# Kernel optimization log

Hardware: AMD Instinct MI355X
Metric: run time of the kernel (lower is better)

Reference implementation:

```python
import jax, jax.numpy as jnp
import numpy as np

N = 65536      # total nodes (512 graphs x 128 agents)
E = 524288     # total edges (avg degree 8)
NPG = 128      # nodes per graph
OBS = 256      # dim_in_node + dim_in_u
HID = 512      # hidden_dim
MID = 256      # dim_mid
LSTM = 256     # dim_lstm_out
DOUT = 128     # dim_out
DLAST = 128    # dim_last
RFM = 256      # rfm_hidden_dim
LH = 256       # last_hidden
ACT = 8        # act_dims


def setup_inputs() -> dict:
    key = jax.random.key(0)
    ks = jax.random.split(key, 30)

    def rn(k, shape, fan_in):
        return jax.random.normal(k, shape, jnp.float32) * (1.0 / np.sqrt(fan_in))

    src = jax.random.randint(ks[3], (E,), 0, N, jnp.int32)
    # keep edges inside each 128-node graph (batched-graph semantics)
    dst = (src // NPG) * NPG + jax.random.randint(ks[4], (E,), 0, NPG, jnp.int32)

    inp = {
        "obs": jax.random.normal(ks[0], (N, OBS), jnp.float32),
        "h0": jax.random.normal(ks[1], (N, LSTM), jnp.float32) * 0.1,
        "c0": jax.random.normal(ks[2], (N, LSTM), jnp.float32) * 0.1,
        "src": src,
        "dst": dst,
        # mlp1a / mlp1b
        "w1a": rn(ks[5], (HID, OBS), OBS), "b1a": jnp.zeros((HID,), jnp.float32),
        "w1b": rn(ks[6], (MID, HID), HID), "b1b": jnp.zeros((MID,), jnp.float32),
        # lstm1 (gate order i,f,g,o as in torch)
        "w_ih": rn(ks[7], (4 * LSTM, MID), MID), "b_ih": jnp.zeros((4 * LSTM,), jnp.float32),
        "w_hh": rn(ks[8], (4 * LSTM, LSTM), LSTM), "b_hh": jnp.zeros((4 * LSTM,), jnp.float32),
        # mlp1
        "w1": rn(ks[9], (DOUT, LSTM), LSTM), "b1": jnp.zeros((DOUT,), jnp.float32),
        # RFMBlock edge MLP (input = src_nf ++ dst_nf = 2*DOUT; edge_feat/u are 0-dim)
        "we": rn(ks[10], (RFM, 2 * DOUT), 2 * DOUT), "be": jnp.zeros((RFM,), jnp.float32),
        "we2": rn(ks[11], (DLAST, RFM), RFM), "be2": jnp.zeros((DLAST,), jnp.float32),
        # RFMBlock node MLP (input = node_feat ++ h = DOUT + DLAST)
        "wn": rn(ks[12], (RFM, DOUT + DLAST), DOUT + DLAST), "bn": jnp.zeros((RFM,), jnp.float32),
        "wn2": rn(ks[13], (DLAST, RFM), RFM), "bn2": jnp.zeros((DLAST,), jnp.float32),
        # readout
        "wr": rn(ks[14], (LH, DLAST), DLAST), "br": jnp.zeros((LH,), jnp.float32),
        "wr2": rn(ks[15], (ACT, LH), LH), "br2": jnp.zeros((ACT,), jnp.float32),
    }
    return inp


def reference(obs, h0, c0, src, dst,
              w1a, b1a, w1b, b1b, w_ih, b_ih, w_hh, b_hh, w1, b1,
              we, be, we2, be2, wn, bn, wn2, bn2, wr, br, wr2, br2):
    # node encoder: mlp1b(relu(mlp1a(obs)))
    x = jnp.maximum(obs @ w1a.T + b1a, 0.0) @ w1b.T + b1b            # [N, MID]
    # single-step LSTM (batch = N nodes, seq_len = 1)
    gates = x @ w_ih.T + h0 @ w_hh.T + (b_ih + b_hh)                 # [N, 4*LSTM]
    i, f, g, o = jnp.split(gates, 4, axis=-1)
    c1 = jax.nn.sigmoid(f) * c0 + jax.nn.sigmoid(i) * jnp.tanh(g)
    h1 = jax.nn.sigmoid(o) * jnp.tanh(c1)
    nf = jnp.maximum(h1, 0.0) @ w1.T + b1                            # [N, DOUT]

    # RFMBlock edge update: fc_edge2(relu(fc_edge([src_nf, dst_nf])))
    einp = jnp.concatenate([nf[src], nf[dst]], axis=-1)              # [E, 2*DOUT]
    ef = jnp.maximum(einp @ we.T + be, 0.0) @ we2.T + be2            # [E, DLAST]

    # message = edge_feat, reduce = sum over incoming edges (by dst)
    agg = jax.ops.segment_sum(ef, dst, num_segments=N)               # [N, DLAST]

    # RFMBlock node update: fc_node2(relu(fc_node([node_feat, h])))
    ninp = jnp.concatenate([nf, agg], axis=-1)                       # [N, DOUT+DLAST]
    nf2 = jnp.maximum(ninp @ wn.T + bn, 0.0) @ wn2.T + bn2           # [N, DLAST]

    # readout: mlp1_readout2(relu(mlp1_readout(n_out)))
    logits = jnp.maximum(nf2 @ wr.T + br, 0.0) @ wr2.T + br2         # [N, ACT]
    return logits, h1, c1
```

## Files before the change

### kernel.cpp

```cpp
#include <hip/hip_runtime.h>
#include <cstdint>
#include <cstddef>


#define NN 65536
#define NE 524288

typedef __bf16 bf16x8 __attribute__((ext_vector_type(8)));
typedef float  f32x4  __attribute__((ext_vector_type(4)));

typedef __attribute__((address_space(1))) unsigned int glb_uint;
typedef __attribute__((address_space(3))) unsigned int lds_uint;

__device__ __forceinline__ void async16(const void* g, void* l){
  __builtin_amdgcn_global_load_lds((glb_uint*)g, (lds_uint*)l, 16, 0, 0);
}

__device__ __forceinline__ float bf2f(unsigned short u){
  union { unsigned int i; float f; } v; v.i = ((unsigned int)u) << 16; return v.f;
}
__device__ __forceinline__ unsigned short f2b(float f){
  union { float f; unsigned int i; } v; v.f = f;
  unsigned int r = v.i + 0x7FFFu + ((v.i >> 16) & 1u);
  return (unsigned short)(r >> 16);
}
__device__ __forceinline__ float sigm(float x){ return 1.f/(1.f+__expf(-x)); }

struct ConvArgs {
  const float* s[14];
  unsigned short* d[14];
  int n4[14];
  int cnt;
};

__global__ __launch_bounds__(256) void convert_kernel(ConvArgs a){
  int stride = gridDim.x * blockDim.x;
  int gid = blockIdx.x * blockDim.x + threadIdx.x;
  for (int seg = 0; seg < a.cnt; ++seg){
    const float4* s = (const float4*)a.s[seg];
    ushort4* d = (ushort4*)a.d[seg];
    int n4 = a.n4[seg];
    for (int i = gid; i < n4; i += stride){
      float4 v = s[i];
      ushort4 o; o.x=f2b(v.x); o.y=f2b(v.y); o.z=f2b(v.z); o.w=f2b(v.w);
      d[i] = o;
    }
  }
}

template<int ACT, int RSCALE>
__global__ __launch_bounds__(256) void gemm_kernel(
    const unsigned short* __restrict__ A, int lda,
    const unsigned short* __restrict__ B, int ldb, int K,
    const float* __restrict__ bias,
    const int* __restrict__ rs,
    unsigned short* __restrict__ C, int ldc)
{
  __shared__ alignas(16) unsigned short As[4096];
  __shared__ alignas(16) unsigned short Bs[4096];
  int t = threadIdx.x, wave = t >> 6, lane = t & 63;
  int m0 = blockIdx.x * 128, n0 = blockIdx.y * 128;
  int wr = wave >> 1, wc = wave & 1;

  f32x4 acc[4][4] = {};

  int srow = lane & 15, schunk = lane >> 4;
  const unsigned short* Ap0 = A + (size_t)(m0 + wave * 16 + srow) * lda + schunk * 8;
  const unsigned short* Ap1 = Ap0 + (size_t)64 * lda;
  const unsigned short* Bp0 = B + (size_t)(n0 + wave * 16 + srow) * ldb + schunk * 8;
  const unsigned short* Bp1 = Bp0 + (size_t)64 * ldb;
  unsigned short* AsW0 = &As[(wave)     << 9];
  unsigned short* AsW1 = &As[(wave + 4) << 9];
  unsigned short* BsW0 = &Bs[(wave)     << 9];
  unsigned short* BsW1 = &Bs[(wave + 4) << 9];

  for (int kt = 0; kt < K; kt += 32){
    __syncthreads();
    async16(Ap0 + kt, AsW0);
    async16(Ap1 + kt, AsW1);
    async16(Bp0 + kt, BsW0);
    async16(Bp1 + kt, BsW1);
    __syncthreads();
    int fo = (schunk << 7) + (srow << 3);
    bf16x8 a[4], b[4];
#pragma unroll
    for (int m = 0; m < 4; ++m) a[m] = *(const bf16x8*)&As[((wr * 4 + m) << 9) + fo];
#pragma unroll
    for (int n = 0; n < 4; ++n) b[n] = *(const bf16x8*)&Bs[((wc * 4 + n) << 9) + fo];
#pragma unroll
    for (int m = 0; m < 4; ++m)
#pragma unroll
      for (int n = 0; n < 4; ++n)
        acc[m][n] = __builtin_amdgcn_mfma_f32_16x16x32_bf16(a[m], b[n], acc[m][n], 0, 0, 0);
  }

  int coll = lane & 15, rq = lane >> 4;
#pragma unroll
  for (int n = 0; n < 4; ++n){
    int col = n0 + wc * 64 + n * 16 + coll;
    float bv = bias[col];
#pragma unroll
    for (int m = 0; m < 4; ++m){
#pragma unroll
      for (int r = 0; r < 4; ++r){
        int rrow = m0 + wr * 64 + m * 16 + rq * 4 + r;
        float scale = RSCALE ? (float)rs[rrow] : 1.0f;
        float v = acc[m][n][r] + bv * scale;
        if (ACT) v = fmaxf(v, 0.f);
        C[(size_t)rrow * ldc + col] = f2b(v);
      }
    }
  }
}

__global__ __launch_bounds__(256) void gates_lstm_kernel(
    const unsigned short* __restrict__ Xb,
    const unsigned short* __restrict__ H0b,
    const unsigned short* __restrict__ Wih,
    const unsigned short* __restrict__ Whh,
    const float* __restrict__ b_ih, const float* __restrict__ b_hh,
    const float* __restrict__ c0,
    float* __restrict__ h1o, float* __restrict__ c1o,
    unsigned short* __restrict__ rb)
{
  __shared__ alignas(16) unsigned short As[2048];
  __shared__ alignas(16) unsigned short Bs[4][2048];
  int t = threadIdx.x, wave = t >> 6, lane = t & 63;
  int m0 = blockIdx.x * 64, cb = blockIdx.y * 64;
  int srow = lane & 15, schunk = lane >> 4;

  f32x4 acc[4][4] = {};

  for (int kt = 0; kt < 512; kt += 32){
    const unsigned short* Abase = (kt < 256) ? (Xb + kt) : (H0b + (kt - 256));
    const unsigned short* Wbase = (kt < 256) ? (Wih + kt) : (Whh + (kt - 256));
    __syncthreads();
    async16(Abase + (size_t)(m0 + wave * 16 + srow) * 256 + schunk * 8, &As[wave << 9]);
#pragma unroll
    for (int g = 0; g < 4; ++g){
      async16(Wbase + (size_t)(g * 256 + cb + wave * 16 + srow) * 256 + schunk * 8,
              &Bs[g][wave << 9]);
    }
    __syncthreads();
    bf16x8 a = *(const bf16x8*)&As[(wave << 9) + (schunk << 7) + (srow << 3)];
#pragma unroll
    for (int g = 0; g < 4; ++g){
#pragma unroll
      for (int j = 0; j < 4; ++j){
        bf16x8 b = *(const bf16x8*)&Bs[g][(j << 9) + (schunk << 7) + (srow << 3)];
        acc[g][j] = __builtin_amdgcn_mfma_f32_16x16x32_bf16(a, b, acc[g][j], 0, 0, 0);
      }
    }
  }

  int coll = lane & 15, rq = lane >> 4;
#pragma unroll
  for (int j = 0; j < 4; ++j){
    int col = cb + j * 16 + coll;
    float bi  = b_ih[col]       + b_hh[col];
    float bff = b_ih[256 + col] + b_hh[256 + col];
    float bg  = b_ih[512 + col] + b_hh[512 + col];
    float bo  = b_ih[768 + col] + b_hh[768 + col];
#pragma unroll
    for (int r = 0; r < 4; ++r){
      int node = m0 + wave * 16 + rq * 4 + r;
      size_t off = (size_t)node * 256 + col;
      float iv = sigm(acc[0][j][r] + bi);
      float fv = sigm(acc[1][j][r] + bff);
      float gv = tanhf(acc[2][j][r] + bg);
      float ov = sigm(acc[3][j][r] + bo);
      float cv = fv * c0[off] + iv * gv;
      float hv = ov * tanhf(cv);
      h1o[off] = hv;
      c1o[off] = cv;
      rb[off] = f2b(fmaxf(hv, 0.f));
    }
  }
}

__global__ __launch_bounds__(256) void hist_kernel(
    const int* __restrict__ dst, int* __restrict__ hist)
{
  int e = blockIdx.x * 256 + threadIdx.x;
  atomicAdd(&hist[dst[e]], 1);
}

__global__ __launch_bounds__(256) void scan1_kernel(
    const int* __restrict__ hist, int* __restrict__ offs, int* __restrict__ bsum)
{
  __shared__ int s[256];
  int b = blockIdx.x, t = threadIdx.x;
  int v = hist[b * 256 + t];
  s[t] = v; __syncthreads();
  for (int d = 1; d < 256; d <<= 1){
    int x = (t >= d) ? s[t - d] : 0;
    __syncthreads();
    s[t] += x;
    __syncthreads();
  }
  offs[b * 256 + t] = s[t] - v;
  if (t == 255) bsum[b] = s[255];
}

__global__ __launch_bounds__(256) void scan2_kernel(int* __restrict__ bsum){
  __shared__ int s[256];
  int t = threadIdx.x;
  int v = bsum[t];
  s[t] = v; __syncthreads();
  for (int d = 1; d < 256; d <<= 1){
    int x = (t >= d) ? s[t - d] : 0;
    __syncthreads();
    s[t] += x;
    __syncthreads();
  }
  bsum[t] = s[t] - v;
}

__global__ __launch_bounds__(256) void scan3_kernel(
    int* __restrict__ offs, const int* __restrict__ bsum, int* __restrict__ cursor)
{
  int i = blockIdx.x * 256 + threadIdx.x;
  int v = offs[i] + bsum[blockIdx.x];
  offs[i] = v;
  cursor[i] = v;
}

__global__ __launch_bounds__(256) void scatter_kernel(
    const int* __restrict__ src, const int* __restrict__ dst,
    int* __restrict__ cursor, int* __restrict__ sorted_src)
{
  int e = blockIdx.x * 256 + threadIdx.x;
  int d = dst[e];
  int pos = atomicAdd(&cursor[d], 1);
  sorted_src[pos] = src[e];
}

__global__ __launch_bounds__(256) void edge_agg_kernel(
    const unsigned short* __restrict__ P,
    const unsigned short* __restrict__ Q,
    const int* __restrict__ sorted_src,
    const int* __restrict__ offs,
    const int* __restrict__ cnt,
    unsigned short* __restrict__ Hsum)
{
  int t = threadIdx.x;
  int n = (blockIdx.x << 2) + (t >> 6);
  int lane = t & 63;
  int d0 = lane * 4;
  int off = offs[n], c = cnt[n];
  ushort4 qv = *(const ushort4*)&Q[(size_t)n * 256 + d0];
  float q0 = bf2f(qv.x), q1 = bf2f(qv.y), q2 = bf2f(qv.z), q3 = bf2f(qv.w);
  float a0 = 0.f, a1 = 0.f, a2 = 0.f, a3 = 0.f;
  for (int i = 0; i < c; ++i){
    int s = sorted_src[off + i];
    ushort4 pv = *(const ushort4*)&P[(size_t)s * 256 + d0];
    a0 += fmaxf(bf2f(pv.x) + q0, 0.f);
    a1 += fmaxf(bf2f(pv.y) + q1, 0.f);
    a2 += fmaxf(bf2f(pv.z) + q2, 0.f);
    a3 += fmaxf(bf2f(pv.w) + q3, 0.f);
  }
  ushort4 o; o.x = f2b(a0); o.y = f2b(a1); o.z = f2b(a2); o.w = f2b(a3);
  *(ushort4*)&Hsum[(size_t)n * 256 + d0] = o;
}

__global__ __launch_bounds__(256) void logits_kernel(
    const unsigned short* __restrict__ rh,
    const unsigned short* __restrict__ wr2b,
    const float* __restrict__ br2,
    float* __restrict__ out)
{
  __shared__ alignas(16) unsigned short W[2048];
  int t = threadIdx.x;
  *(uint4*)&W[t * 8] = *(const uint4*)&wr2b[t * 8];
  __syncthreads();
  int node = blockIdx.x * 32 + (t >> 3);
  int o = t & 7;
  const unsigned short* r = rh + (size_t)node * 256;
  float s = br2[o];
#pragma unroll
  for (int k = 0; k < 256; k += 8){
    uint4 av = *(const uint4*)&r[k];
    const unsigned short* ap = (const unsigned short*)&av;
#pragma unroll
    for (int i = 0; i < 8; ++i) s += bf2f(ap[i]) * bf2f(W[o * 256 + k + i]);
  }
  out[(size_t)node * 8 + o] = s;
}

extern "C" void kernel_launch(void* const* d_in, const int* in_sizes, int n_in,
                              void* d_out, int out_size, void* d_ws, size_t ws_size,
                              hipStream_t stream)
{
  (void)in_sizes; (void)n_in; (void)out_size; (void)ws_size;
  const float* obs = (const float*)d_in[0];
  const float* h0  = (const float*)d_in[1];
  const float* c0  = (const float*)d_in[2];
  const int*   src = (const int*)d_in[3];
  const int*   dst = (const int*)d_in[4];
  const float* w1a = (const float*)d_in[5];
  const float* b1a = (const float*)d_in[6];
  const float* w1b = (const float*)d_in[7];
  const float* b1b = (const float*)d_in[8];
  const float* wih = (const float*)d_in[9];
  const float* bih = (const float*)d_in[10];
  const float* whh = (const float*)d_in[11];
  const float* bhh = (const float*)d_in[12];
  const float* w1  = (const float*)d_in[13];
  const float* b1  = (const float*)d_in[14];
  const float* we  = (const float*)d_in[15];
  const float* be  = (const float*)d_in[16];
  const float* we2 = (const float*)d_in[17];
  const float* be2 = (const float*)d_in[18];
  const float* wn  = (const float*)d_in[19];
  const float* bn  = (const float*)d_in[20];
  const float* wn2 = (const float*)d_in[21];
  const float* bn2 = (const float*)d_in[22];
  const float* wr  = (const float*)d_in[23];
  const float* br  = (const float*)d_in[24];
  const float* wr2 = (const float*)d_in[25];
  const float* br2 = (const float*)d_in[26];

  char* ws = (char*)d_ws;
  typedef unsigned short u16;
  u16* w1a_b = (u16*)(ws + 0);
  u16* w1b_b = (u16*)(ws + 262144);
  u16* wih_b = (u16*)(ws + 524288);
  u16* whh_b = (u16*)(ws + 1048576);
  u16* w1_b  = (u16*)(ws + 1572864);
  u16* we_b  = (u16*)(ws + 1638400);
  u16* we2_b = (u16*)(ws + 1769472);
  u16* wn_b  = (u16*)(ws + 1835008);
  u16* wn2_b = (u16*)(ws + 1966080);
  u16* wr_b  = (u16*)(ws + 2031616);
  u16* wr2_b = (u16*)(ws + 2097152);
  float* zbias = (float*)(ws + 2101248);
  int* hist    = (int*)(ws + 2103296);
  int* offs    = (int*)(ws + 2365440);
  int* cursor  = (int*)(ws + 2627584);
  int* bsum    = (int*)(ws + 2889728);
  int* ssrc    = (int*)(ws + 2890752);

  char* RA = ws + 5242880;
  char* RB = ws + 38797312;
  char* RY = ws + 72351744;

  u16* obs_b = (u16*)RA;
  u16* x_b   = (u16*)RA;
  u16* P     = (u16*)RA;
  u16* nf2   = (u16*)RA;
  u16* h0_b  = (u16*)RB;
  u16* Hsum  = (u16*)RB;
  u16* hidn  = (u16*)RB;
  u16* rh    = (u16*)RB;
  u16* y1    = (u16*)RY;
  u16* rb    = (u16*)RY;
  u16* Q     = (u16*)RY;
  u16* ninp  = (u16*)(RY + 33554432);

  float* logits = (float*)d_out;
  float* h1o = logits + (size_t)NN * 8;
  float* c1o = h1o + (size_t)NN * 256;

  (void)hipMemsetAsync(zbias, 0, 2048, stream);
  (void)hipMemsetAsync(hist, 0, 65536 * 4, stream);

  ConvArgs ca;
  const float* ss[13] = {obs, h0, w1a, w1b, wih, whh, w1, we, we2, wn, wn2, wr, wr2};
  u16* dd[13] = {obs_b, h0_b, w1a_b, w1b_b, wih_b, whh_b, w1_b, we_b, we2_b, wn_b, wn2_b, wr_b, wr2_b};
  int nn[13] = {NN*256, NN*256, 512*256, 256*512, 1024*256, 1024*256, 128*256,
                256*256, 128*256, 256*256, 128*256, 256*128, 8*256};
  for (int i = 0; i < 13; ++i){ ca.s[i]=ss[i]; ca.d[i]=dd[i]; ca.n4[i]=nn[i]/4; }
  ca.cnt = 13;
  convert_kernel<<<2048, 256, 0, stream>>>(ca);

  hist_kernel<<<NE/256, 256, 0, stream>>>(dst, hist);
  scan1_kernel<<<256, 256, 0, stream>>>(hist, offs, bsum);
  scan2_kernel<<<1, 256, 0, stream>>>(bsum);
  scan3_kernel<<<256, 256, 0, stream>>>(offs, bsum, cursor);
  scatter_kernel<<<NE/256, 256, 0, stream>>>(src, dst, cursor, ssrc);

  gemm_kernel<1,0><<<dim3(NN/128, 4), 256, 0, stream>>>(obs_b, 256, w1a_b, 256, 256, b1a, nullptr, y1, 512);
  gemm_kernel<0,0><<<dim3(NN/128, 2), 256, 0, stream>>>(y1, 512, w1b_b, 512, 512, b1b, nullptr, x_b, 256);
  gates_lstm_kernel<<<dim3(NN/64, 4), 256, 0, stream>>>(
      x_b, h0_b, wih_b, whh_b, bih, bhh, c0, h1o, c1o, rb);
  gemm_kernel<0,0><<<dim3(NN/128, 1), 256, 0, stream>>>(rb, 256, w1_b, 256, 256, b1, nullptr, ninp, 256);
  gemm_kernel<0,0><<<dim3(NN/128, 2), 256, 0, stream>>>(ninp, 256, we_b, 256, 128, zbias, nullptr, P, 256);
  gemm_kernel<0,0><<<dim3(NN/128, 2), 256, 0, stream>>>(ninp, 256, we_b + 128, 256, 128, be, nullptr, Q, 256);
  edge_agg_kernel<<<NN/4, 256, 0, stream>>>(P, Q, ssrc, offs, hist, Hsum);
  gemm_kernel<0,1><<<dim3(NN/128, 1), 256, 0, stream>>>(Hsum, 256, we2_b, 256, 256, be2, hist, ninp + 128, 256);
  gemm_kernel<1,0><<<dim3(NN/128, 2), 256, 0, stream>>>(ninp, 256, wn_b, 256, 256, bn, nullptr, hidn, 256);
  gemm_kernel<0,0><<<dim3(NN/128, 1), 256, 0, stream>>>(hidn, 256, wn2_b, 256, 256, bn2, nullptr, nf2, 128);
  gemm_kernel<1,0><<<dim3(NN/128, 2), 256, 0, stream>>>(nf2, 128, wr_b, 128, 128, br, nullptr, rh, 256);
  logits_kernel<<<NN/32, 256, 0, stream>>>(rh, wr2_b, br2, logits);
}
```

Before: 935.8 us.

## Double-buffer LDS tiles in GEMM and LSTM gate kernels

Both the generic bf16 GEMM and the fused LSTM-gates kernel now use two LDS buffers. Each iteration issues the async global-to-LDS loads for the next K tile before running the MFMAs on the current one. This cuts the barriers per K step from two to one and lets global load latency overlap with matrix math. The cost is twice the LDS per block, which may lower occupancy. Correctness relies on the single barrier also waiting for the async LDS loads to complete.

```diff
diff --git a/kernel.cpp b/kernel.cpp
--- a/kernel.cpp
+++ b/kernel.cpp
@@ -56,8 +56,8 @@
     const int* __restrict__ rs,
     unsigned short* __restrict__ C, int ldc)
 {
-  __shared__ alignas(16) unsigned short As[4096];
-  __shared__ alignas(16) unsigned short Bs[4096];
+  __shared__ alignas(16) unsigned short As[2][4096];
+  __shared__ alignas(16) unsigned short Bs[2][4096];
   int t = threadIdx.x, wave = t >> 6, lane = t & 63;
   int m0 = blockIdx.x * 128, n0 = blockIdx.y * 128;
   int wr = wave >> 1, wc = wave & 1;
@@ -69,30 +69,37 @@
   const unsigned short* Ap1 = Ap0 + (size_t)64 * lda;
   const unsigned short* Bp0 = B + (size_t)(n0 + wave * 16 + srow) * ldb + schunk * 8;
   const unsigned short* Bp1 = Bp0 + (size_t)64 * ldb;
-  unsigned short* AsW0 = &As[(wave)     << 9];
-  unsigned short* AsW1 = &As[(wave + 4) << 9];
-  unsigned short* BsW0 = &Bs[(wave)     << 9];
-  unsigned short* BsW1 = &Bs[(wave + 4) << 9];
-
-  for (int kt = 0; kt < K; kt += 32){
-    __syncthreads();
-    async16(Ap0 + kt, AsW0);
-    async16(Ap1 + kt, AsW1);
-    async16(Bp0 + kt, BsW0);
-    async16(Bp1 + kt, BsW1);
-    __syncthreads();
-    int fo = (schunk << 7) + (srow << 3);
-    bf16x8 a[4], b[4];
-#pragma unroll
-    for (int m = 0; m < 4; ++m) a[m] = *(const bf16x8*)&As[((wr * 4 + m) << 9) + fo];
-#pragma unroll
-    for (int n = 0; n < 4; ++n) b[n] = *(const bf16x8*)&Bs[((wc * 4 + n) << 9) + fo];
+
+  auto stage = [&](int b, int kt){
+    async16(Ap0 + kt, &As[b][(wave)     << 9]);
+    async16(Ap1 + kt, &As[b][(wave + 4) << 9]);
+    async16(Bp0 + kt, &Bs[b][(wave)     << 9]);
+    async16(Bp1 + kt, &Bs[b][(wave + 4) << 9]);
+  };
+  int fo = (schunk << 7) + (srow << 3);
+  auto compute = [&](int b){
+    bf16x8 av[4], bv[4];
+#pragma unroll
+    for (int m = 0; m < 4; ++m) av[m] = *(const bf16x8*)&As[b][((wr * 4 + m) << 9) + fo];
+#pragma unroll
+    for (int n = 0; n < 4; ++n) bv[n] = *(const bf16x8*)&Bs[b][((wc * 4 + n) << 9) + fo];
 #pragma unroll
     for (int m = 0; m < 4; ++m)
 #pragma unroll
       for (int n = 0; n < 4; ++n)
-        acc[m][n] = __builtin_amdgcn_mfma_f32_16x16x32_bf16(a[m], b[n], acc[m][n], 0, 0, 0);
-  }
+        acc[m][n] = __builtin_amdgcn_mfma_f32_16x16x32_bf16(av[m], bv[n], acc[m][n], 0, 0, 0);
+  };
+
+  stage(0, 0);
+  __syncthreads();
+  int cur = 0;
+  for (int kt = 32; kt < K; kt += 32){
+    stage(cur ^ 1, kt);
+    compute(cur);
+    __syncthreads();
+    cur ^= 1;
+  }
+  compute(cur);
 
   int coll = lane & 15, rq = lane >> 4;
 #pragma unroll
@@ -123,35 +130,46 @@
     float* __restrict__ h1o, float* __restrict__ c1o,
     unsigned short* __restrict__ rb)
 {
-  __shared__ alignas(16) unsigned short As[2048];
-  __shared__ alignas(16) unsigned short Bs[4][2048];
+  __shared__ alignas(16) unsigned short As[2][2048];
+  __shared__ alignas(16) unsigned short Bs[2][4][2048];
   int t = threadIdx.x, wave = t >> 6, lane = t & 63;
   int m0 = blockIdx.x * 64, cb = blockIdx.y * 64;
   int srow = lane & 15, schunk = lane >> 4;
 
   f32x4 acc[4][4] = {};
 
-  for (int kt = 0; kt < 512; kt += 32){
+  auto stage = [&](int b, int kt){
     const unsigned short* Abase = (kt < 256) ? (Xb + kt) : (H0b + (kt - 256));
     const unsigned short* Wbase = (kt < 256) ? (Wih + kt) : (Whh + (kt - 256));
-    __syncthreads();
-    async16(Abase + (size_t)(m0 + wave * 16 + srow) * 256 + schunk * 8, &As[wave << 9]);
+    async16(Abase + (size_t)(m0 + wave * 16 + srow) * 256 + schunk * 8, &As[b][wave << 9]);
+#pragma unroll
+    for (int g = 0; g < 4; ++g)
+      async16(Wbase + (size_t)(g * 256 + cb + wave * 16 + srow) * 256 + schunk * 8,
+              &Bs[b][g][wave << 9]);
+  };
+  int fo = (schunk << 7) + (srow << 3);
+  auto compute = [&](int b){
+    bf16x8 a = *(const bf16x8*)&As[b][(wave << 9) + fo];
 #pragma unroll
     for (int g = 0; g < 4; ++g){
-      async16(Wbase + (size_t)(g * 256 + cb + wave * 16 + srow) * 256 + schunk * 8,
-              &Bs[g][wave << 9]);
-    }
-    __syncthreads();
-    bf16x8 a = *(const bf16x8*)&As[(wave << 9) + (schunk << 7) + (srow << 3)];
-#pragma unroll
-    for (int g = 0; g < 4; ++g){
 #pragma unroll
       for (int j = 0; j < 4; ++j){
-        bf16x8 b = *(const bf16x8*)&Bs[g][(j << 9) + (schunk << 7) + (srow << 3)];
-        acc[g][j] = __builtin_amdgcn_mfma_f32_16x16x32_bf16(a, b, acc[g][j], 0, 0, 0);
+        bf16x8 bb = *(const bf16x8*)&Bs[b][g][(j << 9) + fo];
+        acc[g][j] = __builtin_amdgcn_mfma_f32_16x16x32_bf16(a, bb, acc[g][j], 0, 0, 0);
       }
     }
-  }
+  };
+
+  stage(0, 0);
+  __syncthreads();
+  int cur = 0;
+  for (int kt = 32; kt < 512; kt += 32){
+    stage(cur ^ 1, kt);
+    compute(cur);
+    __syncthreads();
+    cur ^= 1;
+  }
+  compute(cur);
 
   int coll = lane & 15, rq = lane >> 4;
 #pragma unroll
```

Result: no change. 923.7 us (-1.3%).

## Fuse whole per-graph MLP/LSTM/RFM pipeline into one LDS-resident kernel

Applied to the files above, without the earlier changes.

Replaces the chain of tiled GEMM kernels, the LSTM gate kernel, the edge aggregation kernel and the logits kernel with a single kernel. Each 512-thread block processes one 128-node graph and keeps all intermediate activations in a 128 KB LDS pool. Weights are read directly from global memory as MFMA B operands. Edge aggregation gathers source rows from LDS, relying on the batched-graph property that edges stay inside their graph. The goal is to remove the large global round-trips of intermediates and the many launches. The cost is one resident block per CU, no LDS staging or double buffering of weights, and many block-wide barriers.

```diff
diff --git a/kernel.cpp b/kernel.cpp
--- a/kernel.cpp
+++ b/kernel.cpp
@@ -8,13 +8,6 @@
 
 typedef __bf16 bf16x8 __attribute__((ext_vector_type(8)));
 typedef float  f32x4  __attribute__((ext_vector_type(4)));
-
-typedef __attribute__((address_space(1))) unsigned int glb_uint;
-typedef __attribute__((address_space(3))) unsigned int lds_uint;
-
-__device__ __forceinline__ void async16(const void* g, void* l){
-  __builtin_amdgcn_global_load_lds((glb_uint*)g, (lds_uint*)l, 16, 0, 0);
-}
 
 __device__ __forceinline__ float bf2f(unsigned short u){
   union { unsigned int i; float f; } v; v.i = ((unsigned int)u) << 16; return v.f;
@@ -48,136 +41,6 @@
   }
 }
 
-template<int ACT, int RSCALE>
-__global__ __launch_bounds__(256) void gemm_kernel(
-    const unsigned short* __restrict__ A, int lda,
-    const unsigned short* __restrict__ B, int ldb, int K,
-    const float* __restrict__ bias,
-    const int* __restrict__ rs,
-    unsigned short* __restrict__ C, int ldc)
-{
-  __shared__ alignas(16) unsigned short As[4096];
-  __shared__ alignas(16) unsigned short Bs[4096];
-  int t = threadIdx.x, wave = t >> 6, lane = t & 63;
-  int m0 = blockIdx.x * 128, n0 = blockIdx.y * 128;
-  int wr = wave >> 1, wc = wave & 1;
-
-  f32x4 acc[4][4] = {};
-
-  int srow = lane & 15, schunk = lane >> 4;
-  const unsigned short* Ap0 = A + (size_t)(m0 + wave * 16 + srow) * lda + schunk * 8;
-  const unsigned short* Ap1 = Ap0 + (size_t)64 * lda;
-  const unsigned short* Bp0 = B + (size_t)(n0 + wave * 16 + srow) * ldb + schunk * 8;
-  const unsigned short* Bp1 = Bp0 + (size_t)64 * ldb;
-  unsigned short* AsW0 = &As[(wave)     << 9];
-  unsigned short* AsW1 = &As[(wave + 4) << 9];
-  unsigned short* BsW0 = &Bs[(wave)     << 9];
-  unsigned short* BsW1 = &Bs[(wave + 4) << 9];
-
-  for (int kt = 0; kt < K; kt += 32){
-    __syncthreads();
-    async16(Ap0 + kt, AsW0);
-    async16(Ap1 + kt, AsW1);
-    async16(Bp0 + kt, BsW0);
-    async16(Bp1 + kt, BsW1);
-    __syncthreads();
-    int fo = (schunk << 7) + (srow << 3);
-    bf16x8 a[4], b[4];
-#pragma unroll
-    for (int m = 0; m < 4; ++m) a[m] = *(const bf16x8*)&As[((wr * 4 + m) << 9) + fo];
-#pragma unroll
-    for (int n = 0; n < 4; ++n) b[n] = *(const bf16x8*)&Bs[((wc * 4 + n) << 9) + fo];
-#pragma unroll
-    for (int m = 0; m < 4; ++m)
-#pragma unroll
-      for (int n = 0; n < 4; ++n)
-        acc[m][n] = __builtin_amdgcn_mfma_f32_16x16x32_bf16(a[m], b[n], acc[m][n], 0, 0, 0);
-  }
-
-  int coll = lane & 15, rq = lane >> 4;
-#pragma unroll
-  for (int n = 0; n < 4; ++n){
-    int col = n0 + wc * 64 + n * 16 + coll;
-    float bv = bias[col];
-#pragma unroll
-    for (int m = 0; m < 4; ++m){
-#pragma unroll
-      for (int r = 0; r < 4; ++r){
-        int rrow = m0 + wr * 64 + m * 16 + rq * 4 + r;
-        float scale = RSCALE ? (float)rs[rrow] : 1.0f;
-        float v = acc[m][n][r] + bv * scale;
-        if (ACT) v = fmaxf(v, 0.f);
-        C[(size_t)rrow * ldc + col] = f2b(v);
-      }
-    }
-  }
-}
-
-__global__ __launch_bounds__(256) void gates_lstm_kernel(
-    const unsigned short* __restrict__ Xb,
-    const unsigned short* __restrict__ H0b,
-    const unsigned short* __restrict__ Wih,
-    const unsigned short* __restrict__ Whh,
-    const float* __restrict__ b_ih, const float* __restrict__ b_hh,
-    const float* __restrict__ c0,
-    float* __restrict__ h1o, float* __restrict__ c1o,
-    unsigned short* __restrict__ rb)
-{
-  __shared__ alignas(16) unsigned short As[2048];
-  __shared__ alignas(16) unsigned short Bs[4][2048];
-  int t = threadIdx.x, wave = t >> 6, lane = t & 63;
-  int m0 = blockIdx.x * 64, cb = blockIdx.y * 64;
-  int srow = lane & 15, schunk = lane >> 4;
-
-  f32x4 acc[4][4] = {};
-
-  for (int kt = 0; kt < 512; kt += 32){
-    const unsigned short* Abase = (kt < 256) ? (Xb + kt) : (H0b + (kt - 256));
-    const unsigned short* Wbase = (kt < 256) ? (Wih + kt) : (Whh + (kt - 256));
-    __syncthreads();
-    async16(Abase + (size_t)(m0 + wave * 16 + srow) * 256 + schunk * 8, &As[wave << 9]);
-#pragma unroll
-    for (int g = 0; g < 4; ++g){
-      async16(Wbase + (size_t)(g * 256 + cb + wave * 16 + srow) * 256 + schunk * 8,
-              &Bs[g][wave << 9]);
-    }
-    __syncthreads();
-    bf16x8 a = *(const bf16x8*)&As[(wave << 9) + (schunk << 7) + (srow << 3)];
-#pragma unroll
-    for (int g = 0; g < 4; ++g){
-#pragma unroll
-      for (int j = 0; j < 4; ++j){
-        bf16x8 b = *(const bf16x8*)&Bs[g][(j << 9) + (schunk << 7) + (srow << 3)];
-        acc[g][j] = __builtin_amdgcn_mfma_f32_16x16x32_bf16(a, b, acc[g][j], 0, 0, 0);
-      }
-    }
-  }
-
-  int coll = lane & 15, rq = lane >> 4;
-#pragma unroll
-  for (int j = 0; j < 4; ++j){
-    int col = cb + j * 16 + coll;
-    float bi  = b_ih[col]       + b_hh[col];
-    float bff = b_ih[256 + col] + b_hh[256 + col];
-    float bg  = b_ih[512 + col] + b_hh[512 + col];
-    float bo  = b_ih[768 + col] + b_hh[768 + col];
-#pragma unroll
-    for (int r = 0; r < 4; ++r){
-      int node = m0 + wave * 16 + rq * 4 + r;
-      size_t off = (size_t)node * 256 + col;
-      float iv = sigm(acc[0][j][r] + bi);
-      float fv = sigm(acc[1][j][r] + bff);
-      float gv = tanhf(acc[2][j][r] + bg);
-      float ov = sigm(acc[3][j][r] + bo);
-      float cv = fv * c0[off] + iv * gv;
-      float hv = ov * tanhf(cv);
-      h1o[off] = hv;
-      c1o[off] = cv;
-      rb[off] = f2b(fmaxf(hv, 0.f));
-    }
-  }
-}
-
 __global__ __launch_bounds__(256) void hist_kernel(
     const int* __restrict__ dst, int* __restrict__ hist)
 {
@@ -235,56 +98,445 @@
   sorted_src[pos] = src[e];
 }
 
-__global__ __launch_bounds__(256) void edge_agg_kernel(
-    const unsigned short* __restrict__ P,
-    const unsigned short* __restrict__ Q,
-    const int* __restrict__ sorted_src,
-    const int* __restrict__ offs,
-    const int* __restrict__ cnt,
-    unsigned short* __restrict__ Hsum)
+#define POOL_X   0
+#define POOL_NF  0
+#define POOL_NF2 0
+#define POOL_P   16384
+#define POOL_AGG 16384
+#define POOL_YC  32768
+#define POOL_RB  32768
+#define POOL_Q   32768
+#define POOL_HS  49152
+#define POOL_HID 32768
+#define POOL_RH  32768
+
+__global__ __launch_bounds__(512, 2) void fused_kernel(
+    const unsigned short* __restrict__ obs_b,
+    const unsigned short* __restrict__ h0_b,
+    const float* __restrict__ c0,
+    const unsigned short* __restrict__ w1a_b,
+    const float* __restrict__ b1a,
+    const unsigned short* __restrict__ w1b_b,
+    const float* __restrict__ b1b,
+    const unsigned short* __restrict__ wih_b,
+    const unsigned short* __restrict__ whh_b,
+    const float* __restrict__ b_ih, const float* __restrict__ b_hh,
+    const unsigned short* __restrict__ w1_b,
+    const float* __restrict__ b1,
+    const unsigned short* __restrict__ we_b,
+    const float* __restrict__ be,
+    const unsigned short* __restrict__ we2_b,
+    const float* __restrict__ be2,
+    const unsigned short* __restrict__ wn_b,
+    const float* __restrict__ bn,
+    const unsigned short* __restrict__ wn2_b,
+    const float* __restrict__ bn2,
+    const unsigned short* __restrict__ wr_b,
+    const float* __restrict__ br,
+    const unsigned short* __restrict__ wr2_b,
+    const float* __restrict__ br2,
+    const int* __restrict__ hist, const int* __restrict__ offs,
+    const int* __restrict__ ssrc,
+    float* __restrict__ logits, float* __restrict__ h1o, float* __restrict__ c1o)
 {
-  int t = threadIdx.x;
-  int n = (blockIdx.x << 2) + (t >> 6);
-  int lane = t & 63;
-  int d0 = lane * 4;
-  int off = offs[n], c = cnt[n];
-  ushort4 qv = *(const ushort4*)&Q[(size_t)n * 256 + d0];
-  float q0 = bf2f(qv.x), q1 = bf2f(qv.y), q2 = bf2f(qv.z), q3 = bf2f(qv.w);
-  float a0 = 0.f, a1 = 0.f, a2 = 0.f, a3 = 0.f;
-  for (int i = 0; i < c; ++i){
-    int s = sorted_src[off + i];
-    ushort4 pv = *(const ushort4*)&P[(size_t)s * 256 + d0];
-    a0 += fmaxf(bf2f(pv.x) + q0, 0.f);
-    a1 += fmaxf(bf2f(pv.y) + q1, 0.f);
-    a2 += fmaxf(bf2f(pv.z) + q2, 0.f);
-    a3 += fmaxf(bf2f(pv.w) + q3, 0.f);
-  }
-  ushort4 o; o.x = f2b(a0); o.y = f2b(a1); o.z = f2b(a2); o.w = f2b(a3);
-  *(ushort4*)&Hsum[(size_t)n * 256 + d0] = o;
-}
-
-__global__ __launch_bounds__(256) void logits_kernel(
-    const unsigned short* __restrict__ rh,
-    const unsigned short* __restrict__ wr2b,
-    const float* __restrict__ br2,
-    float* __restrict__ out)
-{
-  __shared__ alignas(16) unsigned short W[2048];
-  int t = threadIdx.x;
-  *(uint4*)&W[t * 8] = *(const uint4*)&wr2b[t * 8];
+  __shared__ alignas(16) unsigned short pool[65536];
+
+  int tid = threadIdx.x;
+  int w = tid >> 6, lane = tid & 63;
+  int wr = w >> 2, wc = w & 3;
+  int l15 = lane & 15, l4 = lane >> 4;
+  int g = blockIdx.x;
+  int gbase = g << 7;
+
+  auto ldA_gb = [&](const unsigned short* base, int rt, int ks) -> bf16x8 {
+    return *(const bf16x8*)(base + (size_t)(gbase + (rt << 4) + l15) * 256 + (ks << 5) + (l4 << 3));
+  };
+  auto ldB = [&](const unsigned short* W, int ldw, int n0, int ks) -> bf16x8 {
+    return *(const bf16x8*)(W + (size_t)(n0 + l15) * ldw + (ks << 5) + (l4 << 3));
+  };
+  auto ldA_tf256 = [&](int base, int rt, int ks) -> bf16x8 {
+    return *(const bf16x8*)&pool[base + (rt << 12) + (((ks << 2) + l4) << 7) + (l15 << 3)];
+  };
+  auto ldA_tf128 = [&](int base, int rt, int ks) -> bf16x8 {
+    return *(const bf16x8*)&pool[base + (rt << 11) + (((ks << 2) + l4) << 7) + (l15 << 3)];
+  };
+  auto stTF256 = [&](int base, int row, int col, unsigned short v){
+    pool[base + ((row >> 4) << 12) + ((col >> 3) << 7) + ((row & 15) << 3) + (col & 7)] = v;
+  };
+  auto stTF128 = [&](int base, int row, int col, unsigned short v){
+    pool[base + ((row >> 4) << 11) + ((col >> 3) << 7) + ((row & 15) << 3) + (col & 7)] = v;
+  };
+
+  {
+    f32x4 xacc[2][4][2] = {};
+    for (int c = 0; c < 4; ++c){
+      f32x4 yacc[4][2] = {};
+#pragma unroll
+      for (int ks = 0; ks < 8; ++ks){
+        bf16x8 a[4];
+#pragma unroll
+        for (int m = 0; m < 4; ++m) a[m] = ldA_gb(obs_b, (wr << 2) + m, ks);
+#pragma unroll
+        for (int n = 0; n < 2; ++n){
+          bf16x8 b = ldB(w1a_b, 256, c * 128 + (wc << 5) + (n << 4), ks);
+#pragma unroll
+          for (int m = 0; m < 4; ++m)
+            yacc[m][n] = __builtin_amdgcn_mfma_f32_16x16x32_bf16(a[m], b, yacc[m][n], 0, 0, 0);
+        }
+      }
+#pragma unroll
+      for (int n = 0; n < 2; ++n){
+        float bv = b1a[c * 128 + (wc << 5) + (n << 4) + l15];
+#pragma unroll
+        for (int m = 0; m < 4; ++m)
+#pragma unroll
+          for (int r = 0; r < 4; ++r){
+            int row = (wr << 6) + (m << 4) + (l4 << 2) + r;
+            int col = (wc << 5) + (n << 4) + l15;
+            stTF128(POOL_YC, row, col, f2b(fmaxf(yacc[m][n][r] + bv, 0.f)));
+          }
+      }
+      __syncthreads();
+#pragma unroll
+      for (int ks = 0; ks < 4; ++ks){
+        bf16x8 a[4];
+#pragma unroll
+        for (int m = 0; m < 4; ++m) a[m] = ldA_tf128(POOL_YC, (wr << 2) + m, ks);
+#pragma unroll
+        for (int nt = 0; nt < 2; ++nt)
+#pragma unroll
+          for (int n = 0; n < 2; ++n){
+            bf16x8 b = ldB(w1b_b, 512, nt * 128 + (wc << 5) + (n << 4), c * 4 + ks);
+#pragma unroll
+            for (int m = 0; m < 4; ++m)
+              xacc[nt][m][n] = __builtin_amdgcn_mfma_f32_16x16x32_bf16(a[m], b, xacc[nt][m][n], 0, 0, 0);
+          }
+      }
+      __syncthreads();
+    }
+#pragma unroll
+    for (int nt = 0; nt < 2; ++nt)
+#pragma unroll
+      for (int n = 0; n < 2; ++n){
+        int col = nt * 128 + (wc << 5) + (n << 4) + l15;
+        float bv = b1b[col];
+#pragma unroll
+        for (int m = 0; m < 4; ++m)
+#pragma unroll
+          for (int r = 0; r < 4; ++r){
+            int row = (wr << 6) + (m << 4) + (l4 << 2) + r;
+            stTF256(POOL_X, row, col, f2b(xacc[nt][m][n][r] + bv));
+          }
+      }
+  }
   __syncthreads();
-  int node = blockIdx.x * 32 + (t >> 3);
-  int o = t & 7;
-  const unsigned short* r = rh + (size_t)node * 256;
-  float s = br2[o];
-#pragma unroll
-  for (int k = 0; k < 256; k += 8){
-    uint4 av = *(const uint4*)&r[k];
-    const unsigned short* ap = (const unsigned short*)&av;
-#pragma unroll
-    for (int i = 0; i < 8; ++i) s += bf2f(ap[i]) * bf2f(W[o * 256 + k + i]);
-  }
-  out[(size_t)node * 8 + o] = s;
+
+  for (int cc = 0; cc < 2; ++cc){
+    f32x4 gacc[4][4][2] = {};
+#pragma unroll
+    for (int ks = 0; ks < 16; ++ks){
+      bf16x8 a[4];
+      const unsigned short* Wb;
+      int krel;
+      if (ks < 8){
+#pragma unroll
+        for (int m = 0; m < 4; ++m) a[m] = ldA_tf256(POOL_X, (wr << 2) + m, ks);
+        Wb = wih_b; krel = ks;
+      } else {
+#pragma unroll
+        for (int m = 0; m < 4; ++m) a[m] = ldA_gb(h0_b, (wr << 2) + m, ks - 8);
+        Wb = whh_b; krel = ks - 8;
+      }
+#pragma unroll
+      for (int gg = 0; gg < 4; ++gg)
+#pragma unroll
+        for (int n = 0; n < 2; ++n){
+          bf16x8 b = ldB(Wb, 256, gg * 256 + cc * 128 + (wc << 5) + (n << 4), krel);
+#pragma unroll
+          for (int m = 0; m < 4; ++m)
+            gacc[gg][m][n] = __builtin_amdgcn_mfma_f32_16x16x32_bf16(a[m], b, gacc[gg][m][n], 0, 0, 0);
+        }
+    }
+#pragma unroll
+    for (int n = 0; n < 2; ++n){
+      int col = cc * 128 + (wc << 5) + (n << 4) + l15;
+      float bi  = b_ih[col]       + b_hh[col];
+      float bff = b_ih[256 + col] + b_hh[256 + col];
+      float bg  = b_ih[512 + col] + b_hh[512 + col];
+      float bo  = b_ih[768 + col] + b_hh[768 + col];
+#pragma unroll
+      for (int m = 0; m < 4; ++m)
+#pragma unroll
+        for (int r = 0; r < 4; ++r){
+          int row = (wr << 6) + (m << 4) + (l4 << 2) + r;
+          size_t off = (size_t)(gbase + row) * 256 + col;
+          float iv = sigm(gacc[0][m][n][r] + bi);
+          float fv = sigm(gacc[1][m][n][r] + bff);
+          float gv = tanhf(gacc[2][m][n][r] + bg);
+          float ov = sigm(gacc[3][m][n][r] + bo);
+          float cv = fv * c0[off] + iv * gv;
+          float hv = ov * tanhf(cv);
+          h1o[off] = hv;
+          c1o[off] = cv;
+          stTF256(POOL_RB, row, col, f2b(fmaxf(hv, 0.f)));
+        }
+    }
+  }
+  __syncthreads();
+
+  {
+    f32x4 acc[4][2] = {};
+#pragma unroll
+    for (int ks = 0; ks < 8; ++ks){
+      bf16x8 a[4];
+#pragma unroll
+      for (int m = 0; m < 4; ++m) a[m] = ldA_tf256(POOL_RB, (wr << 2) + m, ks);
+#pragma unroll
+      for (int n = 0; n < 2; ++n){
+        bf16x8 b = ldB(w1_b, 256, (wc << 5) + (n << 4), ks);
+#pragma unroll
+        for (int m = 0; m < 4; ++m)
+          acc[m][n] = __builtin_amdgcn_mfma_f32_16x16x32_bf16(a[m], b, acc[m][n], 0, 0, 0);
+      }
+    }
+#pragma unroll
+    for (int n = 0; n < 2; ++n){
+      int col = (wc << 5) + (n << 4) + l15;
+      float bv = b1[col];
+#pragma unroll
+      for (int m = 0; m < 4; ++m)
+#pragma unroll
+        for (int r = 0; r < 4; ++r){
+          int row = (wr << 6) + (m << 4) + (l4 << 2) + r;
+          stTF128(POOL_NF, row, col, f2b(acc[m][n][r] + bv));
+        }
+    }
+  }
+  __syncthreads();
+
+  f32x4 agg_acc[4][2] = {};
+  for (int h = 0; h < 2; ++h){
+    {
+      f32x4 pacc[4][2] = {}, qacc[4][2] = {};
+#pragma unroll
+      for (int ks = 0; ks < 4; ++ks){
+        bf16x8 a[4];
+#pragma unroll
+        for (int m = 0; m < 4; ++m) a[m] = ldA_tf128(POOL_NF, (wr << 2) + m, ks);
+#pragma unroll
+        for (int n = 0; n < 2; ++n){
+          bf16x8 bp = ldB(we_b, 256, h * 128 + (wc << 5) + (n << 4), ks);
+          bf16x8 bq = ldB(we_b, 256, h * 128 + (wc << 5) + (n << 4), ks + 4);
+#pragma unroll
+          for (int m = 0; m < 4; ++m){
+            pacc[m][n] = __builtin_amdgcn_mfma_f32_16x16x32_bf16(a[m], bp, pacc[m][n], 0, 0, 0);
+            qacc[m][n] = __builtin_amdgcn_mfma_f32_16x16x32_bf16(a[m], bq, qacc[m][n], 0, 0, 0);
+          }
+        }
+      }
+#pragma unroll
+      for (int n = 0; n < 2; ++n){
+        int col = (wc << 5) + (n << 4) + l15;
+        float bv = be[h * 128 + col];
+#pragma unroll
+        for (int m = 0; m < 4; ++m)
+#pragma unroll
+          for (int r = 0; r < 4; ++r){
+            int row = (wr << 6) + (m << 4) + (l4 << 2) + r;
+            pool[POOL_P + row * 128 + col] = f2b(pacc[m][n][r]);
+            pool[POOL_Q + row * 128 + col] = f2b(qacc[m][n][r] + bv);
+          }
+      }
+    }
+    __syncthreads();
+    {
+      int hl = lane >> 5, ll = lane & 31;
+      int d0 = ll << 2;
+#pragma unroll 1
+      for (int pass = 0; pass < 8; ++pass){
+        int ln = (pass << 4) + (w << 1) + hl;
+        int ng = gbase + ln;
+        int eoff = offs[ng], ecnt = hist[ng];
+        unsigned long long qv = *(const unsigned long long*)&pool[POOL_Q + ln * 128 + d0];
+        float q0 = bf2f((unsigned short)qv);
+        float q1 = bf2f((unsigned short)(qv >> 16));
+        float q2 = bf2f((unsigned short)(qv >> 32));
+        float q3 = bf2f((unsigned short)(qv >> 48));
+        float s0 = 0.f, s1 = 0.f, s2 = 0.f, s3 = 0.f;
+        for (int i = 0; i < ecnt; ++i){
+          int s = ssrc[eoff + i] - gbase;
+          unsigned long long pv = *(const unsigned long long*)&pool[POOL_P + s * 128 + d0];
+          s0 += fmaxf(bf2f((unsigned short)pv) + q0, 0.f);
+          s1 += fmaxf(bf2f((unsigned short)(pv >> 16)) + q1, 0.f);
+          s2 += fmaxf(bf2f((unsigned short)(pv >> 32)) + q2, 0.f);
+          s3 += fmaxf(bf2f((unsigned short)(pv >> 48)) + q3, 0.f);
+        }
+        unsigned long long hv = (unsigned long long)f2b(s0)
+                              | ((unsigned long long)f2b(s1) << 16)
+                              | ((unsigned long long)f2b(s2) << 32)
+                              | ((unsigned long long)f2b(s3) << 48);
+        *(unsigned long long*)&pool[POOL_HS + ((ln >> 4) << 11) + ((d0 >> 3) << 7) + ((ln & 15) << 3) + (d0 & 7)] = hv;
+      }
+    }
+    __syncthreads();
+#pragma unroll
+    for (int ks = 0; ks < 4; ++ks){
+      bf16x8 a[4];
+#pragma unroll
+      for (int m = 0; m < 4; ++m) a[m] = ldA_tf128(POOL_HS, (wr << 2) + m, ks);
+#pragma unroll
+      for (int n = 0; n < 2; ++n){
+        bf16x8 b = ldB(we2_b, 256, (wc << 5) + (n << 4), h * 4 + ks);
+#pragma unroll
+        for (int m = 0; m < 4; ++m)
+          agg_acc[m][n] = __builtin_amdgcn_mfma_f32_16x16x32_bf16(a[m], b, agg_acc[m][n], 0, 0, 0);
+      }
+    }
+    __syncthreads();
+  }
+#pragma unroll
+  for (int n = 0; n < 2; ++n){
+    int col = (wc << 5) + (n << 4) + l15;
+    float bv = be2[col];
+#pragma unroll
+    for (int m = 0; m < 4; ++m)
+#pragma unroll
+      for (int r = 0; r < 4; ++r){
+        int row = (wr << 6) + (m << 4) + (l4 << 2) + r;
+        float dv = (float)hist[gbase + row];
+        stTF128(POOL_AGG, row, col, f2b(agg_acc[m][n][r] + bv * dv));
+      }
+  }
+  __syncthreads();
+
+  {
+    f32x4 hacc[2][4][2] = {};
+#pragma unroll
+    for (int ks = 0; ks < 8; ++ks){
+      bf16x8 a[4];
+      if (ks < 4){
+#pragma unroll
+        for (int m = 0; m < 4; ++m) a[m] = ldA_tf128(POOL_NF, (wr << 2) + m, ks);
+      } else {
+#pragma unroll
+        for (int m = 0; m < 4; ++m) a[m] = ldA_tf128(POOL_AGG, (wr << 2) + m, ks - 4);
+      }
+#pragma unroll
+      for (int nt = 0; nt < 2; ++nt)
+#pragma unroll
+        for (int n = 0; n < 2; ++n){
+          bf16x8 b = ldB(wn_b, 256, nt * 128 + (wc << 5) + (n << 4), ks);
+#pragma unroll
+          for (int m = 0; m < 4; ++m)
+            hacc[nt][m][n] = __builtin_amdgcn_mfma_f32_16x16x32_bf16(a[m], b, hacc[nt][m][n], 0, 0, 0);
+        }
+    }
+    __syncthreads();
+#pragma unroll
+    for (int nt = 0; nt < 2; ++nt)
+#pragma unroll
+      for (int n = 0; n < 2; ++n){
+        int col = nt * 128 + (wc << 5) + (n << 4) + l15;
+        float bv = bn[col];
+#pragma unroll
+        for (int m = 0; m < 4; ++m)
+#pragma unroll
+          for (int r = 0; r < 4; ++r){
+            int row = (wr << 6) + (m << 4) + (l4 << 2) + r;
+            stTF256(POOL_HID, row, col, f2b(fmaxf(hacc[nt][m][n][r] + bv, 0.f)));
+          }
+      }
+  }
+  __syncthreads();
+
+  {
+    f32x4 acc[4][2] = {};
+#pragma unroll
+    for (int ks = 0; ks < 8; ++ks){
+      bf16x8 a[4];
+#pragma unroll
+      for (int m = 0; m < 4; ++m) a[m] = ldA_tf256(POOL_HID, (wr << 2) + m, ks);
+#pragma unroll
+      for (int n = 0; n < 2; ++n){
+        bf16x8 b = ldB(wn2_b, 256, (wc << 5) + (n << 4), ks);
+#pragma unroll
+        for (int m = 0; m < 4; ++m)
+          acc[m][n] = __builtin_amdgcn_mfma_f32_16x16x32_bf16(a[m], b, acc[m][n], 0, 0, 0);
+      }
+    }
+    __syncthreads();
+#pragma unroll
+    for (int n = 0; n < 2; ++n){
+      int col = (wc << 5) + (n << 4) + l15;
+      float bv = bn2[col];
+#pragma unroll
+      for (int m = 0; m < 4; ++m)
+#pragma unroll
+        for (int r = 0; r < 4; ++r){
+          int row = (wr << 6) + (m << 4) + (l4 << 2) + r;
+          stTF128(POOL_NF2, row, col, f2b(acc[m][n][r] + bv));
+        }
+    }
+  }
+  __syncthreads();
+
+  {
+    f32x4 racc[2][4][2] = {};
+#pragma unroll
+    for (int ks = 0; ks < 4; ++ks){
+      bf16x8 a[4];
+#pragma unroll
+      for (int m = 0; m < 4; ++m) a[m] = ldA_tf128(POOL_NF2, (wr << 2) + m, ks);
+#pragma unroll
+      for (int nt = 0; nt < 2; ++nt)
+#pragma unroll
+        for (int n = 0; n < 2; ++n){
+          bf16x8 b = ldB(wr_b, 128, nt * 128 + (wc << 5) + (n << 4), ks);
+#pragma unroll
+          for (int m = 0; m < 4; ++m)
+            racc[nt][m][n] = __builtin_amdgcn_mfma_f32_16x16x32_bf16(a[m], b, racc[nt][m][n], 0, 0, 0);
+        }
+    }
+    __syncthreads();
+#pragma unroll
+    for (int nt = 0; nt < 2; ++nt)
+#pragma unroll
+      for (int n = 0; n < 2; ++n){
+        int col = nt * 128 + (wc << 5) + (n << 4) + l15;
+        float bv = br[col];
+#pragma unroll
+        for (int m = 0; m < 4; ++m)
+#pragma unroll
+          for (int r = 0; r < 4; ++r){
+            int row = (wr << 6) + (m << 4) + (l4 << 2) + r;
+            stTF256(POOL_RH, row, col, f2b(fmaxf(racc[nt][m][n][r] + bv, 0.f)));
+          }
+      }
+  }
+  __syncthreads();
+
+  {
+    int node = tid >> 2, q = tid & 3;
+    int o0 = q << 1;
+    float s0 = br2[o0], s1 = br2[o0 + 1];
+    const unsigned short* w0 = wr2_b + (size_t)o0 * 256;
+    const unsigned short* w1 = w0 + 256;
+#pragma unroll
+    for (int kc = 0; kc < 32; ++kc){
+      const unsigned short* rp = &pool[POOL_RH + ((node >> 4) << 12) + (kc << 7) + ((node & 15) << 3)];
+      const unsigned short* wp0 = w0 + kc * 8;
+      const unsigned short* wp1 = w1 + kc * 8;
+#pragma unroll
+      for (int i = 0; i < 8; ++i){
+        float rv = bf2f(rp[i]);
+        s0 += rv * bf2f(wp0[i]);
+        s1 += rv * bf2f(wp1[i]);
+      }
+    }
+    size_t ob = (size_t)(gbase + node) * 8 + o0;
+    logits[ob] = s0;
+    logits[ob + 1] = s1;
+  }
 }
 
 extern "C" void kernel_launch(void* const* d_in, const int* in_sizes, int n_in,
@@ -333,35 +585,19 @@
   u16* wn2_b = (u16*)(ws + 1966080);
   u16* wr_b  = (u16*)(ws + 2031616);
   u16* wr2_b = (u16*)(ws + 2097152);
-  float* zbias = (float*)(ws + 2101248);
   int* hist    = (int*)(ws + 2103296);
   int* offs    = (int*)(ws + 2365440);
   int* cursor  = (int*)(ws + 2627584);
   int* bsum    = (int*)(ws + 2889728);
   int* ssrc    = (int*)(ws + 2890752);
 
-  char* RA = ws + 5242880;
-  char* RB = ws + 38797312;
-  char* RY = ws + 72351744;
-
-  u16* obs_b = (u16*)RA;
-  u16* x_b   = (u16*)RA;
-  u16* P     = (u16*)RA;
-  u16* nf2   = (u16*)RA;
-  u16* h0_b  = (u16*)RB;
-  u16* Hsum  = (u16*)RB;
-  u16* hidn  = (u16*)RB;
-  u16* rh    = (u16*)RB;
-  u16* y1    = (u16*)RY;
-  u16* rb    = (u16*)RY;
-  u16* Q     = (u16*)RY;
-  u16* ninp  = (u16*)(RY + 33554432);
+  u16* obs_b = (u16*)(ws + 5242880);
+  u16* h0_b  = (u16*)(ws + 38797312);
 
   float* logits = (float*)d_out;
   float* h1o = logits + (size_t)NN * 8;
   float* c1o = h1o + (size_t)NN * 256;
 
-  (void)hipMemsetAsync(zbias, 0, 2048, stream);
   (void)hipMemsetAsync(hist, 0, 65536 * 4, stream);
 
   ConvArgs ca;
@@ -379,17 +615,14 @@
   scan3_kernel<<<256, 256, 0, stream>>>(offs, bsum, cursor);
   scatter_kernel<<<NE/256, 256, 0, stream>>>(src, dst, cursor, ssrc);
 
-  gemm_kernel<1,0><<<dim3(NN/128, 4), 256, 0, stream>>>(obs_b, 256, w1a_b, 256, 256, b1a, nullptr, y1, 512);
-  gemm_kernel<0,0><<<dim3(NN/128, 2), 256, 0, stream>>>(y1, 512, w1b_b, 512, 512, b1b, nullptr, x_b, 256);
-  gates_lstm_kernel<<<dim3(NN/64, 4), 256, 0, stream>>>(
-      x_b, h0_b, wih_b, whh_b, bih, bhh, c0, h1o, c1o, rb);
-  gemm_kernel<0,0><<<dim3(NN/128, 1), 256, 0, stream>>>(rb, 256, w1_b, 256, 256, b1, nullptr, ninp, 256);
-  gemm_kernel<0,0><<<dim3(NN/128, 2), 256, 0, stream>>>(ninp, 256, we_b, 256, 128, zbias, nullptr, P, 256);
-  gemm_kernel<0,0><<<dim3(NN/128, 2), 256, 0, stream>>>(ninp, 256, we_b + 128, 256, 128, be, nullptr, Q, 256);
-  edge_agg_kernel<<<NN/4, 256, 0, stream>>>(P, Q, ssrc, offs, hist, Hsum);
-  gemm_kernel<0,1><<<dim3(NN/128, 1), 256, 0, stream>>>(Hsum, 256, we2_b, 256, 256, be2, hist, ninp + 128, 256);
-  gemm_kernel<1,0><<<dim3(NN/128, 2), 256, 0, stream>>>(ninp, 256, wn_b, 256, 256, bn, nullptr, hidn, 256);
-  gemm_kernel<0,0><<<dim3(NN/128, 1), 256, 0, stream>>>(hidn, 256, wn2_b, 256, 256, bn2, nullptr, nf2, 128);
-  gemm_kernel<1,0><<<dim3(NN/128, 2), 256, 0, stream>>>(nf2, 128, wr_b, 128, 128, br, nullptr, rh, 256);
-  logits_kernel<<<NN/32, 256, 0, stream>>>(rh, wr2_b, br2, logits);
-}
+  fused_kernel<<<NN/128, 512, 0, stream>>>(
+      obs_b, h0_b, c0,
+      w1a_b, b1a, w1b_b, b1b,
+      wih_b, whh_b, bih, bhh,
+      w1_b, b1,
+      we_b, be, we2_b, be2,
+      wn_b, bn, wn2_b, bn2,
+      wr_b, br, wr2_b, br2,
+      hist, offs, ssrc,
+      logits, h1o, c1o);
+}
```

Result: slower. 1.049 ms (+12.1%).
